# Performance work log

Hardware: AMD Instinct MI355X
Metric: run time of the kernel (lower is better)

Reference implementation:

```python
import jax, jax.numpy as jnp
import numpy as np

NEG_SLOPE = 0.2  # GAT LeakyReLU slope
EPS = 1e-16


def _pagat_conv(x, path_index, W, a, b, heads, out_ch, concat):
    """Path-augmented GAT conv: attention over (head, mid, tail) path triples,
    messages flow tail -> head, softmax-normalized per destination node."""
    N = x.shape[0]
    head, mid, tail = path_index[0], path_index[1], path_index[2]
    h = (x @ W).reshape(N, heads, out_ch)            # [N, H, C]
    # attention logits from all three path positions: [P, H]
    e = (jnp.einsum('phc,hc->ph', h[head], a[0])
         + jnp.einsum('phc,hc->ph', h[mid], a[1])
         + jnp.einsum('phc,hc->ph', h[tail], a[2]))
    e = jax.nn.leaky_relu(e, NEG_SLOPE)
    # segment softmax over paths grouped by destination (head) node
    m = jax.ops.segment_max(e, head, num_segments=N)  # [N, H]
    ex = jnp.exp(e - m[head])
    s = jax.ops.segment_sum(ex, head, num_segments=N)  # [N, H]
    alpha = ex / (s[head] + EPS)                       # [P, H]
    # aggregate tail features weighted by attention
    out = jax.ops.segment_sum(alpha[..., None] * h[tail], head, num_segments=N)  # [N, H, C]
    if concat:
        out = out.reshape(N, heads * out_ch)
    else:
        out = out.mean(axis=1)
    return out + b


def setup_inputs() -> dict:
    key = jax.random.key(0)
    ks = jax.random.split(key, 8)
    N, F_in, H, C, CLS, P = 100000, 500, 8, 16, 16, 1000000
    x = jax.random.normal(ks[0], (N, F_in), dtype=jnp.float32)
    path_index = jax.random.randint(ks[1], (3, P), 0, N, dtype=jnp.int32)
    W1 = jax.random.normal(ks[2], (F_in, H * C), dtype=jnp.float32) * 0.05
    a1 = jax.random.normal(ks[3], (3, H, C), dtype=jnp.float32) * 0.05
    b1 = jnp.zeros((H * C,), dtype=jnp.float32)
    W2 = jax.random.normal(ks[4], (H * C, CLS), dtype=jnp.float32) * 0.05
    a2 = jax.random.normal(ks[5], (3, 1, CLS), dtype=jnp.float32) * 0.05
    b2 = jnp.zeros((CLS,), dtype=jnp.float32)
    return {"x": x, "path_index": path_index, "W1": W1, "a1": a1, "b1": b1,
            "W2": W2, "a2": a2, "b2": b2}


def reference(x, path_index, W1, a1, b1, W2, a2, b2):
    # eval mode: dropout is identity
    h = _pagat_conv(x, path_index, W1, a1, b1, heads=8, out_ch=16, concat=True)
    h = jax.nn.elu(h)
    h = _pagat_conv(h, path_index, W2, a2, b2, heads=1, out_ch=16, concat=False)
    return jax.nn.log_softmax(h, axis=1)
```

## Files before the change

kernel.cpp:

```cpp
#include <hip/hip_runtime.h>
#include <hip/hip_bf16.h>

#define F_IN  500
#define HC    128
#define NHEAD 8
#define CDIM  16
#define NCLS  16
#define KPAD  512

static __device__ __forceinline__ float bf(const __hip_bfloat16 v) {
    return __bfloat162float(v);
}

static __device__ __forceinline__ unsigned int enc_f32(float f) {
    unsigned int u = __float_as_uint(f);
    return (u & 0x80000000u) ? ~u : (u | 0x80000000u);
}
static __device__ __forceinline__ float dec_f32(unsigned int u) {
    return __uint_as_float((u & 0x80000000u) ? (u & 0x7FFFFFFFu) : ~u);
}

typedef __bf16 bf16x8 __attribute__((ext_vector_type(8)));
typedef float f32x4 __attribute__((ext_vector_type(4)));

static __device__ __forceinline__ void gload16(const void* g, void* l) {
    __builtin_amdgcn_global_load_lds(
        (const __attribute__((address_space(1))) void*)g,
        (__attribute__((address_space(3))) void*)l, 16, 0, 0);
}

__global__ void zero_i32(int* __restrict__ p, int n) {
    int i = blockIdx.x * blockDim.x + threadIdx.x;
    if (i < n) p[i] = 0;
}

__global__ void transpose_w1(const float* __restrict__ W1,
                             __bf16* __restrict__ w1t_hi,
                             __bf16* __restrict__ w1t_lo)
{
    int id = blockIdx.x * 256 + threadIdx.x;
    int c = id >> 9, k = id & 511;
    float v = (k < F_IN) ? W1[k * HC + c] : 0.f;
    __bf16 h = (__bf16)v;
    w1t_hi[id] = h;
    w1t_lo[id] = (__bf16)(v - (float)h);
}

static __device__ __forceinline__ void split8(const float4 a, const float4 b,
                                              bf16x8& hi, bf16x8& lo) {
    float v[8] = {a.x, a.y, a.z, a.w, b.x, b.y, b.z, b.w};
#pragma unroll
    for (int j = 0; j < 8; j++) {
        __bf16 h = (__bf16)v[j];
        hi[j] = h;
        lo[j] = (__bf16)(v[j] - (float)h);
    }
}

__global__ __launch_bounds__(256, 3) void gemm1_v2(
    const float* __restrict__ x,
    const __bf16* __restrict__ w1hi, const __bf16* __restrict__ w1lo,
    const float* __restrict__ zpad,
    __hip_bfloat16* __restrict__ h1, int N)
{
    __shared__ float As[2][64 * 32];
    __shared__ __bf16 BsH[2][128 * 32];
    __shared__ __bf16 BsL[2][128 * 32];

    const int tid = threadIdx.x;
    const int lane = tid & 63, wave = tid >> 6;
    const int m = lane & 15, q = lane >> 4;
    const int wr = wave >> 1, wc = wave & 1;
    const int n0 = blockIdx.x * 64;
    const int woff = (tid >> 6) << 10;

    auto stage = [&](int buf, int t) {
        const int k0 = t * 32;
#pragma unroll
        for (int j = 0; j < 2; ++j) {
            int idx = j * 256 + tid;
            {
                int r = idx >> 3, ps = idx & 7;
                int ls = ps ^ (r & 7);
                int kk = k0 + ls * 4;
                int grow = n0 + r;
                const float* src = (kk < F_IN)
                    ? (x + (size_t)(grow < N ? grow : 0) * F_IN + kk)
                    : zpad;
                gload16(src, (char*)&As[buf][0] + j * 4096 + woff);
            }
            {
                int c = idx >> 2, ps2 = idx & 3;
                int ls2 = ps2 ^ (c & 3);
                const __bf16* sh = w1hi + c * KPAD + k0 + ls2 * 8;
                const __bf16* sl = w1lo + c * KPAD + k0 + ls2 * 8;
                gload16(sh, (char*)&BsH[buf][0] + j * 4096 + woff);
                gload16(sl, (char*)&BsL[buf][0] + j * 4096 + woff);
            }
        }
    };

    f32x4 acc[2][4];
#pragma unroll
    for (int rt = 0; rt < 2; ++rt)
#pragma unroll
        for (int ct = 0; ct < 4; ++ct) acc[rt][ct] = (f32x4){0.f, 0.f, 0.f, 0.f};

    stage(0, 0);
    __syncthreads();
    int cur = 0;

#pragma unroll 2
    for (int t = 0; t < 16; ++t) {
        if (t < 15) stage(cur ^ 1, t + 1);

        bf16x8 ah[2], al[2];
#pragma unroll
        for (int rt = 0; rt < 2; ++rt) {
            int r = wr * 32 + rt * 16 + m;
            int x7 = r & 7;
            const float4* rowp = (const float4*)&As[cur][r * 32];
            float4 f0 = rowp[(2 * q) ^ x7];
            float4 f1 = rowp[(2 * q + 1) ^ x7];
            split8(f0, f1, ah[rt], al[rt]);
        }
        bf16x8 bh[4], bl[4];
#pragma unroll
        for (int ct = 0; ct < 4; ++ct) {
            int c = wc * 64 + ct * 16 + m;
            int s = q ^ (c & 3);
            bh[ct] = *(const bf16x8*)&BsH[cur][c * 32 + s * 8];
            bl[ct] = *(const bf16x8*)&BsL[cur][c * 32 + s * 8];
        }
#pragma unroll
        for (int rt = 0; rt < 2; ++rt)
#pragma unroll
            for (int ct = 0; ct < 4; ++ct) {
                acc[rt][ct] = __builtin_amdgcn_mfma_f32_16x16x32_bf16(ah[rt], bh[ct], acc[rt][ct], 0, 0, 0);
                acc[rt][ct] = __builtin_amdgcn_mfma_f32_16x16x32_bf16(ah[rt], bl[ct], acc[rt][ct], 0, 0, 0);
                acc[rt][ct] = __builtin_amdgcn_mfma_f32_16x16x32_bf16(al[rt], bh[ct], acc[rt][ct], 0, 0, 0);
            }
        __syncthreads();
        cur ^= 1;
    }

#pragma unroll
    for (int rt = 0; rt < 2; ++rt) {
        int rbase = n0 + wr * 32 + rt * 16 + q * 4;
#pragma unroll
        for (int ct = 0; ct < 4; ++ct) {
            int col = wc * 64 + ct * 16 + m;
#pragma unroll
            for (int r = 0; r < 4; ++r) {
                int row = rbase + r;
                if (row < N)
                    h1[(size_t)row * HC + col] = __float2bfloat16(acc[rt][ct][r]);
            }
        }
    }
}

__global__ void dots1_kernel(const __hip_bfloat16* __restrict__ h1,
                             const float* __restrict__ a1,
                             float* __restrict__ d1, int N)
{
    int id = blockIdx.x * blockDim.x + threadIdx.x;
    if (id >= N * NHEAD) return;
    int n = id >> 3, h = id & 7;
    const __hip_bfloat16* hp = h1 + (size_t)n * HC + h * CDIM;
    float s0 = 0.f, s1 = 0.f, s2 = 0.f;
#pragma unroll
    for (int c = 0; c < CDIM; c++) {
        float v = bf(hp[c]);
        s0 += v * a1[(0 * NHEAD + h) * CDIM + c];
        s1 += v * a1[(1 * NHEAD + h) * CDIM + c];
        s2 += v * a1[(2 * NHEAD + h) * CDIM + c];
    }
    d1[id] = s0;
    d1[N * NHEAD + id] = s1;
    d1[2 * N * NHEAD + id] = s2;
}

__global__ void maxred_d1(const float* __restrict__ d1,
                          unsigned int* __restrict__ gmax, int N)
{
    __shared__ unsigned int sm[16];
    if (threadIdx.x < 16) sm[threadIdx.x] = 0;
    __syncthreads();
    int total = 2 * N * NHEAD;
    for (int i = blockIdx.x * blockDim.x + threadIdx.x; i < total;
         i += gridDim.x * blockDim.x) {
        float v = d1[(size_t)N * NHEAD + i];
        int slot = ((i >= N * NHEAD) ? 8 : 0) + (i & 7);
        atomicMax(&sm[slot], enc_f32(v));
    }
    __syncthreads();
    if (threadIdx.x < 16) atomicMax(&gmax[threadIdx.x], sm[threadIdx.x]);
}

__global__ void maxred_d2(const float* __restrict__ d2,
                          unsigned int* __restrict__ gmax2, int N)
{
    __shared__ unsigned int sm[2];
    if (threadIdx.x < 2) sm[threadIdx.x] = 0;
    __syncthreads();
    int total = 2 * N;
    for (int i = blockIdx.x * blockDim.x + threadIdx.x; i < total;
         i += gridDim.x * blockDim.x) {
        float v = d2[N + i];
        atomicMax(&sm[i >= N ? 1 : 0], enc_f32(v));
    }
    __syncthreads();
    if (threadIdx.x < 2) atomicMax(&gmax2[threadIdx.x], sm[threadIdx.x]);
}

__global__ void hist_kernel(const int* __restrict__ pidx, int* __restrict__ deg, int P) {
    int p = blockIdx.x * blockDim.x + threadIdx.x;
    if (p < P) atomicAdd(deg + pidx[p], 1);
}

__global__ void scan1_kernel(const int* __restrict__ deg, int* __restrict__ start,
                             int* __restrict__ bsum, int N) {
    __shared__ int sh[256];
    int i = blockIdx.x * 256 + threadIdx.x;
    int v = (i < N) ? deg[i] : 0;
    sh[threadIdx.x] = v;
    __syncthreads();
#pragma unroll
    for (int off = 1; off < 256; off <<= 1) {
        int x = (threadIdx.x >= off) ? sh[threadIdx.x - off] : 0;
        __syncthreads();
        sh[threadIdx.x] += x;
        __syncthreads();
    }
    if (i < N) start[i] = sh[threadIdx.x] - v;
    if (threadIdx.x == 255) bsum[blockIdx.x] = sh[255];
}

__global__ void scan2_kernel(int* __restrict__ bsum, int nb) {
    __shared__ int sh[512];
    int v = (threadIdx.x < nb) ? bsum[threadIdx.x] : 0;
    sh[threadIdx.x] = v;
    __syncthreads();
#pragma unroll
    for (int off = 1; off < 512; off <<= 1) {
        int x = (threadIdx.x >= off) ? sh[threadIdx.x - off] : 0;
        __syncthreads();
        sh[threadIdx.x] += x;
        __syncthreads();
    }
    if (threadIdx.x < nb) bsum[threadIdx.x] = sh[threadIdx.x] - v;
}

__global__ void scan3_kernel(int* __restrict__ start, const int* __restrict__ bsum, int N) {
    int i = blockIdx.x * 256 + threadIdx.x;
    if (i < N) start[i] += bsum[blockIdx.x];
}

__global__ void scatter_kernel(const int* __restrict__ pidx,
                               const int* __restrict__ start,
                               int* __restrict__ cursor,
                               int* __restrict__ csr, int P) {
    int p = blockIdx.x * blockDim.x + threadIdx.x;
    if (p >= P) return;
    int hd = pidx[p];
    int pos = atomicAdd(cursor + hd, 1);
    csr[start[hd] + pos] = p;
}

__global__ __launch_bounds__(256) void attn1_csr_kernel(
    const int* __restrict__ csr, const int* __restrict__ start,
    const int* __restrict__ deg, const int* __restrict__ pidx,
    const float* __restrict__ d1, const __hip_bfloat16* __restrict__ h1,
    const float* __restrict__ b1, const unsigned int* __restrict__ gmax,
    float* __restrict__ elu_out, int N, int P)
{
    int node = blockIdx.x * 4 + (threadIdx.x >> 6);
    if (node >= N) return;
    int lane = threadIdx.x & 63;
    int h = lane >> 3;
    int s0 = start[node], dg = deg[node];
    const float* d1m = d1 + (size_t)N * NHEAD;
    const float* d1t = d1 + (size_t)2 * N * NHEAD;
    const float dh = d1[node * NHEAD + h];
    float zub = dh + dec_f32(gmax[h]) + dec_f32(gmax[8 + h]);
    const float mxub = zub > 0.f ? zub : 0.2f * zub;

    float acc0 = 0.f, acc1 = 0.f, den = 0.f;
    for (int k0 = 0; k0 < dg; k0 += 8) {
        int kk = k0 + (lane & 7);
        bool valid = kk < dg;
        int p = csr[s0 + (valid ? kk : dg - 1)];
        int mid = pidx[P + p], tl = pidx[2 * P + p];
        float z = dh + d1m[mid * NHEAD + h] + d1t[tl * NHEAD + h];
        float e = z > 0.f ? z : 0.2f * z;
        float ex = valid ? __expf(e - mxub) : 0.f;
        den += ex;
        int kmax = dg - k0; if (kmax > 8) kmax = 8;
        for (int dk = 0; dk < kmax; dk++) {
            int tl_b = __shfl(tl, dk, 8);
            float ex_b = __shfl(ex, dk, 8);
            __hip_bfloat162 v = *(const __hip_bfloat162*)(h1 + (size_t)tl_b * HC + 2 * lane);
            acc0 += ex_b * bf(v.x);
            acc1 += ex_b * bf(v.y);
        }
    }
#pragma unroll
    for (int w = 1; w < 8; w <<= 1) den += __shfl_xor(den, w, 8);

    float inv = 1.f / (den + 1e-16f);
    int j0 = 2 * lane;
    float v0 = acc0 * inv + b1[j0];
    float v1 = acc1 * inv + b1[j0 + 1];
    v0 = v0 > 0.f ? v0 : __expf(v0) - 1.f;
    v1 = v1 > 0.f ? v1 : __expf(v1) - 1.f;
    *(float2*)(elu_out + (size_t)node * HC + j0) = make_float2(v0, v1);
}

__global__ __launch_bounds__(256) void layer2_kernel(
    const float* __restrict__ elu, const float* __restrict__ W2,
    const float* __restrict__ a2,
    float* __restrict__ h2, float* __restrict__ d2, int N)
{
    __shared__ float rows[16][HC + 1];
    __shared__ float h2s[16][NCLS + 1];
    const int n0 = blockIdx.x * 16;
    const int tid = threadIdx.x;
    for (int idx = tid; idx < 16 * HC; idx += 256) {
        int r = idx >> 7, c = idx & 127;
        rows[r][c] = (n0 + r < N) ? elu[(size_t)(n0 + r) * HC + c] : 0.f;
    }
    __syncthreads();
    int ln = tid >> 4, c = tid & 15;
    float acc = 0.f;
#pragma unroll 8
    for (int j = 0; j < HC; j++) acc += rows[ln][j] * W2[j * NCLS + c];
    h2s[ln][c] = acc;
    if (n0 + ln < N) h2[(size_t)(n0 + ln) * NCLS + c] = acc;
    __syncthreads();
    if (tid < 48) {
        int l = tid / 3, j = tid - l * 3;
        if (n0 + l < N) {
            float s = 0.f;
#pragma unroll
            for (int cc = 0; cc < NCLS; cc++) s += h2s[l][cc] * a2[j * NCLS + cc];
            d2[j * N + n0 + l] = s;
        }
    }
}

__global__ __launch_bounds__(256) void attn2_csr_kernel(
    const int* __restrict__ csr, const int* __restrict__ start,
    const int* __restrict__ deg, const int* __restrict__ pidx,
    const float* __restrict__ d2, const float* __restrict__ h2,
    const float* __restrict__ b2, const unsigned int* __restrict__ gmax2,
    float* __restrict__ out, int N, int P)
{
    int node = blockIdx.x * 16 + (threadIdx.x >> 4);
    if (node >= N) return;
    int c = threadIdx.x & 15;
    int s0 = start[node], dg = deg[node];
    const float dh = d2[node];
    const float* d2m = d2 + N;
    const float* d2t = d2 + 2 * N;
    float zub = dh + dec_f32(gmax2[0]) + dec_f32(gmax2[1]);
    const float mxub = zub > 0.f ? zub : 0.2f * zub;

    float acc = 0.f, den = 0.f;
    for (int k0 = 0; k0 < dg; k0 += 16) {
        int kk = k0 + c;
        bool valid = kk < dg;
        int p = csr[s0 + (valid ? kk : dg - 1)];
        int mid = pidx[P + p], tl = pidx[2 * P + p];
        float z = dh + d2m[mid] + d2t[tl];
        float e = z > 0.f ? z : 0.2f * z;
        float ex = valid ? __expf(e - mxub) : 0.f;
        den += ex;
        int kmax = dg - k0; if (kmax > 16) kmax = 16;
        for (int dk = 0; dk < kmax; dk++) {
            int tl_b = __shfl(tl, dk, 16);
            float ex_b = __shfl(ex, dk, 16);
            acc += ex_b * h2[(size_t)tl_b * NCLS + c];
        }
    }
#pragma unroll
    for (int w = 1; w < 16; w <<= 1) den += __shfl_xor(den, w, 16);

    float o = acc / (den + 1e-16f) + b2[c];
    float m2 = o;
#pragma unroll
    for (int w = 1; w < 16; w <<= 1) m2 = fmaxf(m2, __shfl_xor(m2, w, 16));
    float ex = __expf(o - m2), sm = ex;
#pragma unroll
    for (int w = 1; w < 16; w <<= 1) sm += __shfl_xor(sm, w, 16);
    float r = o - m2 - __logf(sm);
    out[(size_t)node * NCLS + c] = r;
}

extern "C" void kernel_launch(void* const* d_in, const int* in_sizes, int n_in,
                              void* d_out, int out_size, void* d_ws, size_t ws_size,
                              hipStream_t stream)
{
    const float* x  = (const float*)d_in[0];
    const int*   pi = (const int*)d_in[1];
    const float* W1 = (const float*)d_in[2];
    const float* a1 = (const float*)d_in[3];
    const float* b1 = (const float*)d_in[4];
    const float* W2 = (const float*)d_in[5];
    const float* a2 = (const float*)d_in[6];
    const float* b2 = (const float*)d_in[7];

    const int N = in_sizes[0] / F_IN;
    const int P = in_sizes[1] / 3;

    float* ws = (float*)d_ws;
    size_t off_h1     = 0;
    size_t off_d1     = (size_t)64 * N;
    size_t off_elu    = (size_t)88 * N;
    size_t off_h2     = (size_t)216 * N;
    size_t off_d2     = (size_t)232 * N;
    size_t off_deg    = (size_t)235 * N;
    size_t off_start  = (size_t)236 * N;
    size_t off_cursor = (size_t)237 * N;
    size_t off_gmax   = (size_t)238 * N;
    size_t off_zpad   = (size_t)238 * N + 32;
    size_t off_bsum   = (size_t)238 * N + 96;
    size_t off_csr    = (size_t)238 * N + 96 + 1024;
    size_t off_w1th   = off_csr + P;
    size_t off_w1tl   = off_w1th + 32768;

    __hip_bfloat16* h1 = (__hip_bfloat16*)(ws + off_h1);
    float* d1   = ws + off_d1;
    float* elu  = ws + off_elu;
    float* h2   = ws + off_h2;
    float* d2   = ws + off_d2;
    int* deg    = (int*)(ws + off_deg);
    int* start  = (int*)(ws + off_start);
    int* cursor = (int*)(ws + off_cursor);
    unsigned int* gmax  = (unsigned int*)(ws + off_gmax);
    unsigned int* gmax2 = (unsigned int*)(ws + off_gmax) + 16;
    float* zpad = ws + off_zpad;
    int* bsum   = (int*)(ws + off_bsum);
    int* csr    = (int*)(ws + off_csr);
    __bf16* w1t_hi = (__bf16*)(ws + off_w1th);
    __bf16* w1t_lo = (__bf16*)(ws + off_w1tl);

    const int BLK = 256;
    const int nb = (N + 255) / 256;

    transpose_w1<<<(HC * KPAD) / 256, 256, 0, stream>>>(W1, w1t_hi, w1t_lo);
    zero_i32<<<(3 * N + 96 + BLK - 1) / BLK, BLK, 0, stream>>>(deg, 3 * N + 96);
    gemm1_v2<<<(N + 63) / 64, 256, 0, stream>>>(x, w1t_hi, w1t_lo, zpad, h1, N);
    dots1_kernel<<<(N * NHEAD + BLK - 1) / BLK, BLK, 0, stream>>>(h1, a1, d1, N);
    maxred_d1<<<1024, 256, 0, stream>>>(d1, gmax, N);
    hist_kernel<<<(P + BLK - 1) / BLK, BLK, 0, stream>>>(pi, deg, P);
    scan1_kernel<<<nb, 256, 0, stream>>>(deg, start, bsum, N);
    scan2_kernel<<<1, 512, 0, stream>>>(bsum, nb);
    scan3_kernel<<<nb, 256, 0, stream>>>(start, bsum, N);
    scatter_kernel<<<(P + BLK - 1) / BLK, BLK, 0, stream>>>(pi, start, cursor, csr, P);
    attn1_csr_kernel<<<(N + 3) / 4, 256, 0, stream>>>(csr, start, deg, pi, d1, h1, b1, gmax, elu, N, P);
    layer2_kernel<<<(N + 15) / 16, 256, 0, stream>>>(elu, W2, a2, h2, d2, N);
    maxred_d2<<<256, 256, 0, stream>>>(d2, gmax2, N);
    attn2_csr_kernel<<<(N + 15) / 16, 256, 0, stream>>>(csr, start, deg, pi, d2, h2, b2, gmax2,
                                                        (float*)d_out, N, P);
}
```

Baseline: 701.3 us.

## Triple-buffer GEMM pipeline, fuse max reductions and prep kernels, unroll gather loops

```diff
diff --git a/kernel.cpp b/kernel.cpp
--- a/kernel.cpp
+++ b/kernel.cpp
@@ -29,21 +29,20 @@
         (__attribute__((address_space(3))) void*)l, 16, 0, 0);
 }
 
-__global__ void zero_i32(int* __restrict__ p, int n) {
-    int i = blockIdx.x * blockDim.x + threadIdx.x;
-    if (i < n) p[i] = 0;
-}
-
-__global__ void transpose_w1(const float* __restrict__ W1,
-                             __bf16* __restrict__ w1t_hi,
-                             __bf16* __restrict__ w1t_lo)
+__global__ void prep_kernel(const float* __restrict__ W1,
+                            __bf16* __restrict__ w1t_hi,
+                            __bf16* __restrict__ w1t_lo,
+                            int* __restrict__ zp, int nz)
 {
     int id = blockIdx.x * 256 + threadIdx.x;
-    int c = id >> 9, k = id & 511;
-    float v = (k < F_IN) ? W1[k * HC + c] : 0.f;
-    __bf16 h = (__bf16)v;
-    w1t_hi[id] = h;
-    w1t_lo[id] = (__bf16)(v - (float)h);
+    if (id < HC * KPAD) {
+        int c = id >> 9, k = id & 511;
+        float v = (k < F_IN) ? W1[k * HC + c] : 0.f;
+        __bf16 h = (__bf16)v;
+        w1t_hi[id] = h;
+        w1t_lo[id] = (__bf16)(v - (float)h);
+    }
+    if (id < nz) zp[id] = 0;
 }
 
 static __device__ __forceinline__ void split8(const float4 a, const float4 b,
@@ -57,22 +56,22 @@
     }
 }
 
-__global__ __launch_bounds__(256, 3) void gemm1_v2(
+__global__ __launch_bounds__(256, 2) void gemm1_v3(
     const float* __restrict__ x,
     const __bf16* __restrict__ w1hi, const __bf16* __restrict__ w1lo,
     const float* __restrict__ zpad,
     __hip_bfloat16* __restrict__ h1, int N)
 {
-    __shared__ float As[2][64 * 32];
-    __shared__ __bf16 BsH[2][128 * 32];
-    __shared__ __bf16 BsL[2][128 * 32];
+    __shared__ float As[3][64 * 32];
+    __shared__ __bf16 BsH[3][128 * 32];
+    __shared__ __bf16 BsL[3][128 * 32];
 
     const int tid = threadIdx.x;
     const int lane = tid & 63, wave = tid >> 6;
     const int m = lane & 15, q = lane >> 4;
     const int wr = wave >> 1, wc = wave & 1;
     const int n0 = blockIdx.x * 64;
-    const int woff = (tid >> 6) << 10;
+    const int woff = wave << 10;
 
     auto stage = [&](int buf, int t) {
         const int k0 = t * 32;
@@ -92,10 +91,8 @@
             {
                 int c = idx >> 2, ps2 = idx & 3;
                 int ls2 = ps2 ^ (c & 3);
-                const __bf16* sh = w1hi + c * KPAD + k0 + ls2 * 8;
-                const __bf16* sl = w1lo + c * KPAD + k0 + ls2 * 8;
-                gload16(sh, (char*)&BsH[buf][0] + j * 4096 + woff);
-                gload16(sl, (char*)&BsL[buf][0] + j * 4096 + woff);
+                gload16(w1hi + c * KPAD + k0 + ls2 * 8, (char*)&BsH[buf][0] + j * 4096 + woff);
+                gload16(w1lo + c * KPAD + k0 + ls2 * 8, (char*)&BsL[buf][0] + j * 4096 + woff);
             }
         }
     };
@@ -107,13 +104,18 @@
         for (int ct = 0; ct < 4; ++ct) acc[rt][ct] = (f32x4){0.f, 0.f, 0.f, 0.f};
 
     stage(0, 0);
-    __syncthreads();
-    int cur = 0;
-
-#pragma unroll 2
+    stage(1, 1);
+
+#pragma unroll
     for (int t = 0; t < 16; ++t) {
-        if (t < 15) stage(cur ^ 1, t + 1);
-
+        if (t > 0) __builtin_amdgcn_s_barrier();
+        if (t + 2 < 16) stage((t + 2) % 3, t + 2);
+        if (t < 14)       asm volatile("s_waitcnt vmcnt(12)" ::: "memory");
+        else if (t == 14) asm volatile("s_waitcnt vmcnt(6)" ::: "memory");
+        else              asm volatile("s_waitcnt vmcnt(0)" ::: "memory");
+        __builtin_amdgcn_s_barrier();
+
+        const int cur = t % 3;
         bf16x8 ah[2], al[2];
 #pragma unroll
         for (int rt = 0; rt < 2; ++rt) {
@@ -132,6 +134,7 @@
             bh[ct] = *(const bf16x8*)&BsH[cur][c * 32 + s * 8];
             bl[ct] = *(const bf16x8*)&BsL[cur][c * 32 + s * 8];
         }
+        __builtin_amdgcn_s_setprio(1);
 #pragma unroll
         for (int rt = 0; rt < 2; ++rt)
 #pragma unroll
@@ -140,8 +143,7 @@
                 acc[rt][ct] = __builtin_amdgcn_mfma_f32_16x16x32_bf16(ah[rt], bl[ct], acc[rt][ct], 0, 0, 0);
                 acc[rt][ct] = __builtin_amdgcn_mfma_f32_16x16x32_bf16(al[rt], bh[ct], acc[rt][ct], 0, 0, 0);
             }
-        __syncthreads();
-        cur ^= 1;
+        __builtin_amdgcn_s_setprio(0);
     }
 
 #pragma unroll
@@ -162,56 +164,32 @@
 
 __global__ void dots1_kernel(const __hip_bfloat16* __restrict__ h1,
                              const float* __restrict__ a1,
-                             float* __restrict__ d1, int N)
-{
-    int id = blockIdx.x * blockDim.x + threadIdx.x;
-    if (id >= N * NHEAD) return;
-    int n = id >> 3, h = id & 7;
-    const __hip_bfloat16* hp = h1 + (size_t)n * HC + h * CDIM;
-    float s0 = 0.f, s1 = 0.f, s2 = 0.f;
-#pragma unroll
-    for (int c = 0; c < CDIM; c++) {
-        float v = bf(hp[c]);
-        s0 += v * a1[(0 * NHEAD + h) * CDIM + c];
-        s1 += v * a1[(1 * NHEAD + h) * CDIM + c];
-        s2 += v * a1[(2 * NHEAD + h) * CDIM + c];
-    }
-    d1[id] = s0;
-    d1[N * NHEAD + id] = s1;
-    d1[2 * N * NHEAD + id] = s2;
-}
-
-__global__ void maxred_d1(const float* __restrict__ d1,
-                          unsigned int* __restrict__ gmax, int N)
+                             float* __restrict__ d1,
+                             unsigned int* __restrict__ gmax, int N)
 {
     __shared__ unsigned int sm[16];
     if (threadIdx.x < 16) sm[threadIdx.x] = 0;
     __syncthreads();
-    int total = 2 * N * NHEAD;
-    for (int i = blockIdx.x * blockDim.x + threadIdx.x; i < total;
-         i += gridDim.x * blockDim.x) {
-        float v = d1[(size_t)N * NHEAD + i];
-        int slot = ((i >= N * NHEAD) ? 8 : 0) + (i & 7);
-        atomicMax(&sm[slot], enc_f32(v));
+    int id = blockIdx.x * blockDim.x + threadIdx.x;
+    if (id < N * NHEAD) {
+        int n = id >> 3, h = id & 7;
+        const __hip_bfloat16* hp = h1 + (size_t)n * HC + h * CDIM;
+        float s0 = 0.f, s1 = 0.f, s2 = 0.f;
+#pragma unroll
+        for (int c = 0; c < CDIM; c++) {
+            float v = bf(hp[c]);
+            s0 += v * a1[(0 * NHEAD + h) * CDIM + c];
+            s1 += v * a1[(1 * NHEAD + h) * CDIM + c];
+            s2 += v * a1[(2 * NHEAD + h) * CDIM + c];
+        }
+        d1[id] = s0;
+        d1[N * NHEAD + id] = s1;
+        d1[2 * N * NHEAD + id] = s2;
+        atomicMax(&sm[h], enc_f32(s1));
+        atomicMax(&sm[8 + h], enc_f32(s2));
     }
     __syncthreads();
     if (threadIdx.x < 16) atomicMax(&gmax[threadIdx.x], sm[threadIdx.x]);
-}
-
-__global__ void maxred_d2(const float* __restrict__ d2,
-                          unsigned int* __restrict__ gmax2, int N)
-{
-    __shared__ unsigned int sm[2];
-    if (threadIdx.x < 2) sm[threadIdx.x] = 0;
-    __syncthreads();
-    int total = 2 * N;
-    for (int i = blockIdx.x * blockDim.x + threadIdx.x; i < total;
-         i += gridDim.x * blockDim.x) {
-        float v = d2[N + i];
-        atomicMax(&sm[i >= N ? 1 : 0], enc_f32(v));
-    }
-    __syncthreads();
-    if (threadIdx.x < 2) atomicMax(&gmax2[threadIdx.x], sm[threadIdx.x]);
 }
 
 __global__ void hist_kernel(const int* __restrict__ pidx, int* __restrict__ deg, int P) {
@@ -296,8 +274,8 @@
         float e = z > 0.f ? z : 0.2f * z;
         float ex = valid ? __expf(e - mxub) : 0.f;
         den += ex;
-        int kmax = dg - k0; if (kmax > 8) kmax = 8;
-        for (int dk = 0; dk < kmax; dk++) {
+#pragma unroll
+        for (int dk = 0; dk < 8; dk++) {
             int tl_b = __shfl(tl, dk, 8);
             float ex_b = __shfl(ex, dk, 8);
             __hip_bfloat162 v = *(const __hip_bfloat162*)(h1 + (size_t)tl_b * HC + 2 * lane);
@@ -320,12 +298,15 @@
 __global__ __launch_bounds__(256) void layer2_kernel(
     const float* __restrict__ elu, const float* __restrict__ W2,
     const float* __restrict__ a2,
-    float* __restrict__ h2, float* __restrict__ d2, int N)
+    float* __restrict__ h2, float* __restrict__ d2,
+    unsigned int* __restrict__ gmax2, int N)
 {
     __shared__ float rows[16][HC + 1];
     __shared__ float h2s[16][NCLS + 1];
+    __shared__ unsigned int smax[2];
     const int n0 = blockIdx.x * 16;
     const int tid = threadIdx.x;
+    if (tid < 2) smax[tid] = 0;
     for (int idx = tid; idx < 16 * HC; idx += 256) {
         int r = idx >> 7, c = idx & 127;
         rows[r][c] = (n0 + r < N) ? elu[(size_t)(n0 + r) * HC + c] : 0.f;
@@ -345,8 +326,11 @@
 #pragma unroll
             for (int cc = 0; cc < NCLS; cc++) s += h2s[l][cc] * a2[j * NCLS + cc];
             d2[j * N + n0 + l] = s;
-        }
-    }
+            if (j) atomicMax(&smax[j - 1], enc_f32(s));
+        }
+    }
+    __syncthreads();
+    if (tid < 2) atomicMax(&gmax2[tid], smax[tid]);
 }
 
 __global__ __launch_bounds__(256) void attn2_csr_kernel(
@@ -376,8 +360,8 @@
         float e = z > 0.f ? z : 0.2f * z;
         float ex = valid ? __expf(e - mxub) : 0.f;
         den += ex;
-        int kmax = dg - k0; if (kmax > 16) kmax = 16;
-        for (int dk = 0; dk < kmax; dk++) {
+#pragma unroll
+        for (int dk = 0; dk < 16; dk++) {
             int tl_b = __shfl(tl, dk, 16);
             float ex_b = __shfl(ex, dk, 16);
             acc += ex_b * h2[(size_t)tl_b * NCLS + c];
@@ -447,20 +431,18 @@
 
     const int BLK = 256;
     const int nb = (N + 255) / 256;
-
-    transpose_w1<<<(HC * KPAD) / 256, 256, 0, stream>>>(W1, w1t_hi, w1t_lo);
-    zero_i32<<<(3 * N + 96 + BLK - 1) / BLK, BLK, 0, stream>>>(deg, 3 * N + 96);
-    gemm1_v2<<<(N + 63) / 64, 256, 0, stream>>>(x, w1t_hi, w1t_lo, zpad, h1, N);
-    dots1_kernel<<<(N * NHEAD + BLK - 1) / BLK, BLK, 0, stream>>>(h1, a1, d1, N);
-    maxred_d1<<<1024, 256, 0, stream>>>(d1, gmax, N);
+    const int nz = 3 * N + 96;
+
+    prep_kernel<<<(nz + 255) / 256, 256, 0, stream>>>(W1, w1t_hi, w1t_lo, deg, nz);
+    gemm1_v3<<<(N + 63) / 64, 256, 0, stream>>>(x, w1t_hi, w1t_lo, zpad, h1, N);
+    dots1_kernel<<<(N * NHEAD + BLK - 1) / BLK, BLK, 0, stream>>>(h1, a1, d1, gmax, N);
     hist_kernel<<<(P + BLK - 1) / BLK, BLK, 0, stream>>>(pi, deg, P);
     scan1_kernel<<<nb, 256, 0, stream>>>(deg, start, bsum, N);
     scan2_kernel<<<1, 512, 0, stream>>>(bsum, nb);
     scan3_kernel<<<nb, 256, 0, stream>>>(start, bsum, N);
     scatter_kernel<<<(P + BLK - 1) / BLK, BLK, 0, stream>>>(pi, start, cursor, csr, P);
     attn1_csr_kernel<<<(N + 3) / 4, 256, 0, stream>>>(csr, start, deg, pi, d1, h1, b1, gmax, elu, N, P);
-    layer2_kernel<<<(N + 15) / 16, 256, 0, stream>>>(elu, W2, a2, h2, d2, N);
-    maxred_d2<<<256, 256, 0, stream>>>(d2, gmax2, N);
+    layer2_kernel<<<(N + 15) / 16, 256, 0, stream>>>(elu, W2, a2, h2, d2, gmax2, N);
     attn2_csr_kernel<<<(N + 15) / 16, 256, 0, stream>>>(csr, start, deg, pi, d2, h2, b2, gmax2,
                                                         (float*)d_out, N, P);
 }
```

Result: slower. 721.0 us (+2.8%).
